# Kernel tuning notes

Measured on AMD Instinct MI355X. Metric: run time of the kernel, lower is better.

Reference implementation:

```python
import jax, jax.numpy as jnp
import numpy as np

N, C, H, D, K = 16384, 256, 8, 64, 8
HID, OUT, NE = 512, 64, 64
COMMIT, RADIUS, RHID = 0.25, 10.0, 16


def setup_inputs() -> dict:
    key = jax.random.key(0)
    ks = jax.random.split(key, 20)
    def w(k, shape, fan_in):
        return jax.random.normal(k, shape, jnp.float32) / np.sqrt(fan_in).astype(np.float32)
    return {
        'x': jax.random.normal(ks[0], (N, C), jnp.float32),
        'coors': jax.random.normal(ks[1], (N, 3), jnp.float32) * 3.0,
        'nbr_idx': jax.random.randint(ks[2], (N, K), 0, N, jnp.int32),
        'Wq': w(ks[3], (C, H * D), C),
        'Wk': w(ks[4], (C, H * D), C),
        'Wv': w(ks[5], (C, H * D), C),
        'w_gate': w(ks[6], (C, H), C),
        'Wr1': w(ks[7], (1, RHID), 1),
        'br1': jnp.zeros((RHID,), jnp.float32),
        'Wr2': w(ks[8], (RHID, H), RHID),
        'br2': jnp.zeros((H,), jnp.float32),
        'Wo': w(ks[9], (H * D + H, C), H * D + H),
        'alpha1': jnp.float32(0.5) * jnp.ones((), jnp.float32),
        'gamma1': jnp.ones((C,), jnp.float32),
        'beta1': jnp.zeros((C,), jnp.float32),
        'Wlin': w(ks[10], (C, HID), C),
        'blin': jnp.zeros((HID,), jnp.float32),
        'alpha2': jnp.float32(0.5) * jnp.ones((), jnp.float32),
        'gamma2': jnp.ones((HID + 20,), jnp.float32),
        'beta2': jnp.zeros((HID + 20,), jnp.float32),
        'Wout': w(ks[11], (HID + 20, OUT), HID + 20),
        'bout': jnp.zeros((OUT,), jnp.float32),
        'codebook': jax.random.normal(ks[12], (NE, OUT), jnp.float32),
    }


def reference(x, coors, Wq, Wk, Wv, w_gate, Wr1, br1, Wr2, br2, Wo,
              alpha1, gamma1, beta1, Wlin, blin, alpha2, gamma2, beta2,
              Wout, bout, codebook, nbr_idx):
    # ---- SE(3)-equivariant sparse-neighbor attention (heads=8, dim_head=64, K=8) ----
    q = (x @ Wq).reshape(N, H, D)
    xn = x[nbr_idx]                                  # [N,K,C] neighbor gather
    k = (xn @ Wk).reshape(N, K, H, D)
    v = (xn @ Wv).reshape(N, K, H, D)
    rel = coors[nbr_idx] - coors[:, None, :]         # [N,K,3]
    dist = jnp.sqrt(jnp.sum(rel * rel, -1) + 1e-8)   # [N,K]
    unit = rel / dist[..., None]
    radial = jax.nn.gelu(dist[..., None] @ Wr1 + br1) @ Wr2 + br2   # [N,K,H]
    logits = jnp.einsum('nhd,nkhd->nkh', q, k) / np.float32(np.sqrt(D)) + radial
    logits = jnp.where((dist <= RADIUS)[..., None], logits, jnp.float32(-1e9))
    attn = jax.nn.softmax(logits, axis=1)            # over K neighbors
    out0 = jnp.einsum('nkh,nkhd->nhd', attn, v).reshape(N, H * D)   # degree-0
    gate = xn @ w_gate                               # [N,K,H]
    vec = jnp.einsum('nkh,nkx->nhx', attn * gate, unit)             # degree-1 [N,H,3]
    vecnorm = jnp.sqrt(jnp.sum(vec * vec, -1) + 1e-8)               # invariant [N,H]
    se3_out = x + jnp.concatenate([out0, vecnorm], -1) @ Wo         # residual
    # ---- lin: DynamicTanh -> Linear -> GELU ----
    h = jnp.tanh(alpha1 * se3_out) * gamma1 + beta1
    h = jax.nn.gelu(h @ Wlin + blin)
    # ---- out_dense: concat 20-dim aa feats, DynamicTanh -> Linear -> GELU -> Tanh ----
    h2 = jnp.concatenate([h, x[:, :20]], -1)
    h2 = jnp.tanh(alpha2 * h2) * gamma2 + beta2
    z = jnp.tanh(jax.nn.gelu(h2 @ Wout + bout))      # [N,OUT]
    # ---- VQ-EMA: nearest codebook entry, commitment loss, straight-through ----
    d2 = (jnp.sum(z * z, -1, keepdims=True)
          - 2.0 * z @ codebook.T
          + jnp.sum(codebook * codebook, -1))
    idx = jnp.argmin(d2, axis=-1)
    zq = codebook[idx]
    vq_loss = COMMIT * jnp.mean((z - jax.lax.stop_gradient(zq)) ** 2)
    z_quantized = z + jax.lax.stop_gradient(zq - z)
    return z_quantized, vq_loss
```

## Files before the change

kernel.cpp:

```cpp
#include <hip/hip_runtime.h>
#include <hip/hip_bf16.h>
#include <stdint.h>

#define NPTS 16384
#define CDIM 256
#define HEADS 8
#define KNBR 8
#define HIDD 512
#define OUTD 64
#define NEMB 64
#define RHIDD 16

typedef _Float16 half8 __attribute__((ext_vector_type(8)));
typedef float f32x4 __attribute__((ext_vector_type(4)));

__device__ __forceinline__ float gelu_tanh(float v) {
    float v3 = v * v * v;
    return 0.5f * v * (1.0f + tanhf(0.79788456080286535588f * (v + 0.044715f * v3)));
}

__device__ __forceinline__ void gload16(const void* g, void* l) {
    __builtin_amdgcn_global_load_lds((const __attribute__((address_space(1))) void*)g,
                                     (__attribute__((address_space(3))) void*)l, 16, 0, 0);
}

template <int EPI>
__launch_bounds__(256)
__global__ void gemm_split(const _Float16* __restrict__ A2, const _Float16* __restrict__ B2,
                           int Kpad, int KT,
                           void* __restrict__ Cout, int ldc,
                           const float* __restrict__ bias,
                           const float* __restrict__ res,
                           const float* __restrict__ alphap,
                           const float* __restrict__ gamma,
                           const float* __restrict__ beta,
                           const float* __restrict__ a2p,
                           const float* __restrict__ g2,
                           const float* __restrict__ b2,
                           void* __restrict__ aux) {
    __shared__ __align__(16) char lds[32768];

    const int tid = threadIdx.x;
    const int l = tid & 63, w = tid >> 6;
    const int g = l >> 4, r = l & 15;
    const int wr = w >> 1, wc = w & 1;
    const int m0 = blockIdx.y * 128;
    const int n0 = blockIdx.x * 128;
    const int ldA = 2 * Kpad;
    const int srow = l >> 3;
    const int scol = ((l & 7) ^ srow) << 3;
    const int swz = (r & 7) << 4;
    const int aBase = (wr * 64 + r) * 128;
    const int bBase = 16384 + (wc * 64 + r) * 128;

    f32x4 acc[4][4] = {};

    for (int kt = 0; kt < KT; ++kt) {
        int k0 = kt * 64;
        int term = (k0 >= Kpad) ? ((k0 >= 2 * Kpad) ? 2 : 1) : 0;
        int kk0 = k0 - term * Kpad;
        int srcA = (term < 2) ? kk0 : (Kpad + kk0);
        int srcB = (term == 1) ? (Kpad + kk0) : kk0;
        const _Float16* aS = A2 + (size_t)m0 * ldA + srcA + scol;
        const _Float16* bS = B2 + (size_t)n0 * ldA + srcB + scol;
        #pragma unroll
        for (int cc = 0; cc < 4; ++cc) {
            int ch = w * 4 + cc;
            int row = ch * 8 + srow;
            gload16(aS + (size_t)row * ldA, lds + ch * 1024);
            gload16(bS + (size_t)row * ldA, lds + 16384 + ch * 1024);
        }
        __syncthreads();
        #pragma unroll
        for (int kb = 0; kb < 2; ++kb) {
            int ko = ((kb << 6) | (g << 4)) ^ swz;
            half8 af[4], bf[4];
            #pragma unroll
            for (int i = 0; i < 4; ++i) af[i] = *(const half8*)(lds + aBase + i * 2048 + ko);
            #pragma unroll
            for (int j = 0; j < 4; ++j) bf[j] = *(const half8*)(lds + bBase + j * 2048 + ko);
            #pragma unroll
            for (int i = 0; i < 4; ++i)
                #pragma unroll
                for (int j = 0; j < 4; ++j)
                    acc[i][j] = __builtin_amdgcn_mfma_f32_16x16x32_f16(af[i], bf[j], acc[i][j], 0, 0, 0);
        }
        __syncthreads();
    }

    const float alp = (EPI == 1 || EPI == 2) ? alphap[0] : 0.f;
    #pragma unroll
    for (int i = 0; i < 4; ++i) {
        #pragma unroll
        for (int j = 0; j < 4; ++j) {
            const int gcol = n0 + wc * 64 + j * 16 + r;
            #pragma unroll
            for (int q = 0; q < 4; ++q) {
                const int row = m0 + wr * 64 + i * 16 + g * 4 + q;
                float v = acc[i][j][q];
                if (EPI == 0) {
                    if (gcol < 1536) {
                        ((float*)Cout)[(size_t)row * 1536 + gcol] = v;
                    } else if (gcol < 1544) {
                        ((float*)aux)[(size_t)row * 8 + (gcol - 1536)] = v;
                    }
                } else if (EPI == 1) {
                    v += res[(size_t)row * CDIM + gcol];
                    v = tanhf(alp * v) * gamma[gcol] + beta[gcol];
                    _Float16 hi = (_Float16)v;
                    _Float16 lo = (_Float16)(v - (float)hi);
                    _Float16* H = (_Float16*)Cout;
                    H[(size_t)row * 512 + gcol] = hi;
                    H[(size_t)row * 512 + 256 + gcol] = lo;
                    if (gcol < 64) {
                        int tc = 512 + gcol;
                        float tv = 0.f;
                        if (gcol < 20)
                            tv = tanhf(a2p[0] * res[(size_t)row * CDIM + gcol]) * g2[tc] + b2[tc];
                        _Float16 thi = (_Float16)tv;
                        _Float16 tlo = (_Float16)(tv - (float)thi);
                        _Float16* T = (_Float16*)aux;
                        T[(size_t)row * 1152 + tc] = thi;
                        T[(size_t)row * 1152 + 576 + tc] = tlo;
                    }
                } else if (EPI == 2) {
                    v = gelu_tanh(v + bias[gcol]);
                    v = tanhf(alp * v) * gamma[gcol] + beta[gcol];
                    _Float16 hi = (_Float16)v;
                    _Float16 lo = (_Float16)(v - (float)hi);
                    _Float16* H = (_Float16*)Cout;
                    H[(size_t)row * 1152 + gcol] = hi;
                    H[(size_t)row * 1152 + 576 + gcol] = lo;
                }
            }
        }
    }
}

__launch_bounds__(256)
__global__ void gemm_out_vq(const _Float16* __restrict__ A2, const _Float16* __restrict__ B2,
                            const float* __restrict__ bout, const float* __restrict__ cb,
                            float* __restrict__ outZ, float* __restrict__ partials) {
    __shared__ __align__(16) char lds[34816];
    __shared__ float psum[64];
    float* zL  = (float*)lds;
    float* cbL = (float*)(lds + 17408);

    const int tid = threadIdx.x;
    const int l = tid & 63, w = tid >> 6;
    const int g = l >> 4, r = l & 15;
    const int wr = w >> 1, wc = w & 1;
    const int m0 = blockIdx.x * 64;
    const int ldA = 1152;
    const int srow = l >> 3;
    const int scol = ((l & 7) ^ srow) << 3;
    const int swz = (r & 7) << 4;
    const int aBase = (wr * 32 + r) * 128;
    const int bBase = 8192 + (wc * 32 + r) * 128;

    f32x4 acc[2][2] = {};

    for (int kt = 0; kt < 27; ++kt) {
        int k0 = kt * 64;
        int term = (k0 >= 576) ? ((k0 >= 1152) ? 2 : 1) : 0;
        int kk0 = k0 - term * 576;
        int srcA = (term < 2) ? kk0 : (576 + kk0);
        int srcB = (term == 1) ? (576 + kk0) : kk0;
        const _Float16* aS = A2 + (size_t)m0 * ldA + srcA + scol;
        const _Float16* bS = B2 + srcB + scol;
        #pragma unroll
        for (int cc = 0; cc < 2; ++cc) {
            int ch = w * 2 + cc;
            int row = ch * 8 + srow;
            gload16(aS + (size_t)row * ldA, lds + ch * 1024);
            gload16(bS + (size_t)row * ldA, lds + 8192 + ch * 1024);
        }
        __syncthreads();
        #pragma unroll
        for (int kb = 0; kb < 2; ++kb) {
            int ko = ((kb << 6) | (g << 4)) ^ swz;
            half8 af[2], bf[2];
            #pragma unroll
            for (int i = 0; i < 2; ++i) af[i] = *(const half8*)(lds + aBase + i * 2048 + ko);
            #pragma unroll
            for (int j = 0; j < 2; ++j) bf[j] = *(const half8*)(lds + bBase + j * 2048 + ko);
            #pragma unroll
            for (int i = 0; i < 2; ++i)
                #pragma unroll
                for (int j = 0; j < 2; ++j)
                    acc[i][j] = __builtin_amdgcn_mfma_f32_16x16x32_f16(af[i], bf[j], acc[i][j], 0, 0, 0);
        }
        __syncthreads();
    }

    #pragma unroll
    for (int i = 0; i < 2; ++i) {
        #pragma unroll
        for (int j = 0; j < 2; ++j) {
            int col = wc * 32 + j * 16 + r;
            #pragma unroll
            for (int q = 0; q < 4; ++q) {
                int rl = wr * 32 + i * 16 + g * 4 + q;
                zL[rl * 68 + col] = tanhf(gelu_tanh(acc[i][j][q] + bout[col]));
            }
        }
    }
    for (int i = tid; i < NEMB * OUTD / 4; i += 256) {
        float4 v = ((const float4*)cb)[i];
        int e = (i * 4) >> 6, c0 = (i * 4) & 63;
        cbL[e * 68 + c0 + 0] = v.x; cbL[e * 68 + c0 + 1] = v.y;
        cbL[e * 68 + c0 + 2] = v.z; cbL[e * 68 + c0 + 3] = v.w;
    }
    __syncthreads();
    if (tid < 64) {
        float cc = 0.f;
        #pragma unroll
        for (int d = 0; d < 64; ++d) { float cv = cbL[tid * 68 + d]; cc += cv * cv; }
        cbL[tid * 68 + 64] = cc;
    }
    __syncthreads();

    const int row = tid >> 2, part = tid & 3;
    float best = 1e30f;
    int bidx = 0;
    for (int e = part * 16; e < part * 16 + 16; ++e) {
        float dot = 0.f;
        #pragma unroll
        for (int d = 0; d < 64; ++d) dot += zL[row * 68 + d] * cbL[e * 68 + d];
        float sc = cbL[e * 68 + 64] - 2.f * dot;
        if (sc < best) { best = sc; bidx = e; }
    }
    #pragma unroll
    for (int m = 1; m <= 2; m <<= 1) {
        float ob = __shfl_xor(best, m, 64);
        int oi = __shfl_xor(bidx, m, 64);
        if (ob < best || (ob == best && oi < bidx)) { best = ob; bidx = oi; }
    }
    const int grow = m0 + row;
    float lsum = 0.f;
    #pragma unroll
    for (int u = 0; u < 16; ++u) {
        float cv = cbL[bidx * 68 + part * 16 + u];
        outZ[(size_t)grow * 64 + part * 16 + u] = cv;
        float df = zL[row * 68 + part * 16 + u] - cv;
        lsum += df * df;
    }
    lsum += __shfl_xor(lsum, 1, 64);
    lsum += __shfl_xor(lsum, 2, 64);
    if (part == 0) psum[row] = lsum;
    __syncthreads();
    if (tid < 64) {
        float v = psum[tid];
        #pragma unroll
        for (int m = 1; m < 64; m <<= 1) v += __shfl_xor(v, m, 64);
        if (tid == 0) partials[blockIdx.x] = v;
    }
}

__global__ void vq_reduce(const float* __restrict__ partials, float* __restrict__ out) {
    __shared__ float s[256];
    int tid = threadIdx.x;
    s[tid] = partials[tid];
    __syncthreads();
    for (int st = 128; st > 0; st >>= 1) {
        if (tid < st) s[tid] += s[tid + st];
        __syncthreads();
    }
    if (tid == 0) out[0] = 0.25f * s[0] / ((float)NPTS * (float)OUTD);
}

#define R0 (NPTS * CDIM)
#define S1 (1664 * 256)
#define S2 (256 * 576)
#define S3 (512 * 256)
#define S4 (64 * 576)
__global__ void prep(const float* __restrict__ x,
                     const float* __restrict__ Wq, const float* __restrict__ Wk,
                     const float* __restrict__ Wv, const float* __restrict__ w_gate,
                     const float* __restrict__ Wo, const float* __restrict__ Wlin,
                     const float* __restrict__ Wout,
                     _Float16* __restrict__ x2, _Float16* __restrict__ wqkv2,
                     _Float16* __restrict__ wo2, _Float16* __restrict__ wlin2,
                     _Float16* __restrict__ wout2) {
    for (int idx = blockIdx.x * 256 + threadIdx.x; idx < R0 + S1 + S2 + S3 + S4;
         idx += gridDim.x * 256) {
        float v; _Float16* dst; size_t o0, o1;
        if (idx < R0) {
            int n = idx >> 8, cc = idx & 255;
            v = x[idx];
            dst = x2; o0 = (size_t)n * 512 + cc; o1 = o0 + 256;
        } else if (idx < R0 + S1) {
            int t = idx - R0;
            int j = t >> 8, k = t & 255;
            if (j < 1536) {
                int jm = j & 511;
                const float* W = (j < 512) ? Wq : (j < 1024) ? Wk : Wv;
                v = W[(size_t)k * 512 + jm];
            } else if (j < 1544) {
                v = w_gate[(size_t)k * 8 + (j - 1536)];
            } else {
                v = 0.f;
            }
            dst = wqkv2; o0 = (size_t)j * 512 + k; o1 = o0 + 256;
        } else if (idx < R0 + S1 + S2) {
            int t = idx - R0 - S1;
            int j = t / 576, k = t - j * 576;
            v = (k < 520) ? Wo[(size_t)k * 256 + j] : 0.f;
            dst = wo2; o0 = (size_t)j * 1152 + k; o1 = o0 + 576;
        } else if (idx < R0 + S1 + S2 + S3) {
            int t = idx - R0 - S1 - S2;
            int j = t >> 8, k = t & 255;
            v = Wlin[(size_t)k * 512 + j];
            dst = wlin2; o0 = (size_t)j * 512 + k; o1 = o0 + 256;
        } else {
            int t = idx - R0 - S1 - S2 - S3;
            int j = t / 576, k = t - j * 576;
            v = (k < 532) ? Wout[(size_t)k * 64 + j] : 0.f;
            dst = wout2; o0 = (size_t)j * 1152 + k; o1 = o0 + 576;
        }
        _Float16 hi = (_Float16)v, lo = (_Float16)(v - (float)hi);
        dst[o0] = hi; dst[o1] = lo;
    }
}

__launch_bounds__(256)
__global__ void attn_kernel(const float* __restrict__ QKV, const float* __restrict__ G,
                            const float* __restrict__ coors, const int* __restrict__ nbr,
                            const float* __restrict__ Wr1, const float* __restrict__ br1,
                            const float* __restrict__ Wr2, const float* __restrict__ br2,
                            _Float16* __restrict__ att2) {
    __shared__ float unitL[4][8][3];
    __shared__ float distL[4][8];
    __shared__ float radH[4][8][16];

    const int tid = threadIdx.x;
    const int w = tid >> 6;
    const int lane = tid & 63;
    const int n = blockIdx.x * 4 + w;
    const int h = lane >> 3;
    const int c = lane & 7;

    int jreg[KNBR];
    #pragma unroll
    for (int k = 0; k < KNBR; ++k) jreg[k] = nbr[(size_t)n * KNBR + k];

    if (lane < KNBR) {
        int jj = jreg[lane];
        float rx = coors[(size_t)jj * 3 + 0] - coors[(size_t)n * 3 + 0];
        float ry = coors[(size_t)jj * 3 + 1] - coors[(size_t)n * 3 + 1];
        float rz = coors[(size_t)jj * 3 + 2] - coors[(size_t)n * 3 + 2];
        float d = sqrtf(rx * rx + ry * ry + rz * rz + 1e-8f);
        float inv = 1.0f / d;
        distL[w][lane] = d;
        unitL[w][lane][0] = rx * inv;
        unitL[w][lane][1] = ry * inv;
        unitL[w][lane][2] = rz * inv;
    }

    const float4* qp = (const float4*)(QKV + (size_t)n * 1536 + lane * 8);
    float4 q0 = qp[0], q1 = qp[1];
    float p[KNBR];
    #pragma unroll
    for (int k = 0; k < KNBR; ++k) {
        const float4* kp = (const float4*)(QKV + (size_t)jreg[k] * 1536 + 512 + lane * 8);
        float4 k0 = kp[0], k1 = kp[1];
        p[k] = q0.x * k0.x + q0.y * k0.y + q0.z * k0.z + q0.w * k0.w
             + q1.x * k1.x + q1.y * k1.y + q1.z * k1.z + q1.w * k1.w;
    }
    #pragma unroll
    for (int m = 1; m <= 4; m <<= 1) {
        #pragma unroll
        for (int k = 0; k < KNBR; ++k) p[k] += __shfl_xor(p[k], m, 64);
    }
    __syncthreads();

    #pragma unroll
    for (int rr = 0; rr < 2; ++rr) {
        int idx = lane + rr * 64;
        int k = idx >> 4, i = idx & 15;
        float hv = distL[w][k] * Wr1[i] + br1[i];
        radH[w][k][i] = gelu_tanh(hv);
    }
    __syncthreads();

    float lg[KNBR];
    float b2v = br2[h];
    #pragma unroll
    for (int k = 0; k < KNBR; ++k) {
        float rad = b2v;
        #pragma unroll
        for (int i = 0; i < RHIDD; ++i) rad += radH[w][k][i] * Wr2[i * HEADS + h];
        lg[k] = p[k] * 0.125f + rad;
        if (!(distL[w][k] <= 10.0f)) lg[k] = -1e9f;
    }
    float mx = lg[0];
    #pragma unroll
    for (int k = 1; k < KNBR; ++k) mx = fmaxf(mx, lg[k]);
    float a[KNBR];
    float s = 0.f;
    #pragma unroll
    for (int k = 0; k < KNBR; ++k) { a[k] = expf(lg[k] - mx); s += a[k]; }
    float is = 1.0f / s;
    #pragma unroll
    for (int k = 0; k < KNBR; ++k) a[k] *= is;

    float vx = 0.f, vy = 0.f, vz = 0.f;
    #pragma unroll
    for (int k = 0; k < KNBR; ++k) {
        float gg = G[(size_t)jreg[k] * HEADS + h];
        float ag = a[k] * gg;
        vx += ag * unitL[w][k][0];
        vy += ag * unitL[w][k][1];
        vz += ag * unitL[w][k][2];
    }
    float vn = sqrtf(vx * vx + vy * vy + vz * vz + 1e-8f);

    float4 o0 = {0.f, 0.f, 0.f, 0.f}, o1 = {0.f, 0.f, 0.f, 0.f};
    #pragma unroll
    for (int k = 0; k < KNBR; ++k) {
        const float4* vp = (const float4*)(QKV + (size_t)jreg[k] * 1536 + 1024 + lane * 8);
        float4 v0 = vp[0], v1 = vp[1];
        float ak = a[k];
        o0.x += ak * v0.x; o0.y += ak * v0.y; o0.z += ak * v0.z; o0.w += ak * v0.w;
        o1.x += ak * v1.x; o1.y += ak * v1.y; o1.z += ak * v1.z; o1.w += ak * v1.w;
    }

    float ov[8] = {o0.x, o0.y, o0.z, o0.w, o1.x, o1.y, o1.z, o1.w};
    half8 hi8, lo8;
    #pragma unroll
    for (int t = 0; t < 8; ++t) {
        _Float16 hi = (_Float16)ov[t];
        hi8[t] = hi;
        lo8[t] = (_Float16)(ov[t] - (float)hi);
    }
    *(half8*)(att2 + (size_t)n * 1152 + lane * 8) = hi8;
    *(half8*)(att2 + (size_t)n * 1152 + 576 + lane * 8) = lo8;
    if (c == 0) {
        _Float16 hi = (_Float16)vn, lo = (_Float16)(vn - (float)hi);
        att2[(size_t)n * 1152 + 512 + h] = hi;
        att2[(size_t)n * 1152 + 576 + 512 + h] = lo;
    }
    if (lane < 56) {
        att2[(size_t)n * 1152 + 520 + lane] = (_Float16)0.f;
        att2[(size_t)n * 1152 + 1096 + lane] = (_Float16)0.f;
    }
}

extern "C" void kernel_launch(void* const* d_in, const int* in_sizes, int n_in,
                              void* d_out, int out_size, void* d_ws, size_t ws_size,
                              hipStream_t stream) {
    const float* x      = (const float*)d_in[0];
    const float* coors  = (const float*)d_in[1];
    const int*   nbr    = (const int*)  d_in[2];
    const float* Wq     = (const float*)d_in[3];
    const float* Wk     = (const float*)d_in[4];
    const float* Wv     = (const float*)d_in[5];
    const float* w_gate = (const float*)d_in[6];
    const float* Wr1    = (const float*)d_in[7];
    const float* br1    = (const float*)d_in[8];
    const float* Wr2    = (const float*)d_in[9];
    const float* br2    = (const float*)d_in[10];
    const float* Wo     = (const float*)d_in[11];
    const float* alpha1 = (const float*)d_in[12];
    const float* gamma1 = (const float*)d_in[13];
    const float* beta1  = (const float*)d_in[14];
    const float* Wlin   = (const float*)d_in[15];
    const float* blin   = (const float*)d_in[16];
    const float* alpha2 = (const float*)d_in[17];
    const float* gamma2 = (const float*)d_in[18];
    const float* beta2  = (const float*)d_in[19];
    const float* Wout   = (const float*)d_in[20];
    const float* bout   = (const float*)d_in[21];
    const float* cb     = (const float*)d_in[22];

    char* wsb = (char*)d_ws;
    float*    QKV   = (float*)   (wsb + 0);
    _Float16* att2  = (_Float16*)(wsb + 100663296);
    _Float16* x2    = (_Float16*)(wsb + 138412032);
    _Float16* wqkv2 = (_Float16*)(wsb + 155189248);
    _Float16* wo2   = (_Float16*)(wsb + 156893184);
    _Float16* wlin2 = (_Float16*)(wsb + 157483008);
    _Float16* wout2 = (_Float16*)(wsb + 158007296);
    float*    G     = (float*)   (wsb + 158154752);
    float*    part  = (float*)   (wsb + 158679040);
    _Float16* h1s   = (_Float16*)(wsb + 0);
    _Float16* h2s   = (_Float16*)(wsb + 20299776);

    float* outZ    = (float*)d_out;
    float* outLoss = outZ + (size_t)NPTS * OUTD;

    dim3 blk(256);

    prep<<<dim3(2048), blk, 0, stream>>>(x, Wq, Wk, Wv, w_gate, Wo, Wlin, Wout,
                                         x2, wqkv2, wo2, wlin2, wout2);
    gemm_split<0><<<dim3(13, 128), blk, 0, stream>>>(x2, wqkv2, 256, 12, QKV, 1536,
        nullptr, nullptr, nullptr, nullptr, nullptr, nullptr, nullptr, nullptr, G);
    attn_kernel<<<dim3(NPTS / 4), blk, 0, stream>>>(QKV, G, coors, nbr, Wr1, br1, Wr2, br2, att2);
    gemm_split<1><<<dim3(2, 128), blk, 0, stream>>>(att2, wo2, 576, 27, h1s, 0,
        nullptr, x, alpha1, gamma1, beta1, alpha2, gamma2, beta2, h2s);
    gemm_split<2><<<dim3(4, 128), blk, 0, stream>>>(h1s, wlin2, 256, 12, h2s, 0,
        blin, nullptr, alpha2, gamma2, beta2, nullptr, nullptr, nullptr, nullptr);
    gemm_out_vq<<<dim3(256), blk, 0, stream>>>(h2s, wout2, bout, cb, outZ, part);
    vq_reduce<<<dim3(1), blk, 0, stream>>>(part, outLoss);
}
```

Measured before the change: 426.8 us.

## Load hi and lo split-fp16 halves into one tile and reuse fragments

```diff
diff --git a/kernel.cpp b/kernel.cpp
--- a/kernel.cpp
+++ b/kernel.cpp
@@ -48,43 +48,53 @@
     const int n0 = blockIdx.x * 128;
     const int ldA = 2 * Kpad;
     const int srow = l >> 3;
-    const int scol = ((l & 7) ^ srow) << 3;
-    const int swz = (r & 7) << 4;
+    const int sl = (l & 7) ^ srow;
+    const int scol = (sl & 3) * 8 + ((sl >= 4) ? Kpad : 0);
+    const int swz = (l & 7) << 4;
     const int aBase = (wr * 64 + r) * 128;
     const int bBase = 16384 + (wc * 64 + r) * 128;
+    const int koh = (g << 4) ^ swz;
+    const int kol = (64 | (g << 4)) ^ swz;
 
     f32x4 acc[4][4] = {};
 
-    for (int kt = 0; kt < KT; ++kt) {
-        int k0 = kt * 64;
-        int term = (k0 >= Kpad) ? ((k0 >= 2 * Kpad) ? 2 : 1) : 0;
-        int kk0 = k0 - term * Kpad;
-        int srcA = (term < 2) ? kk0 : (Kpad + kk0);
-        int srcB = (term == 1) ? (Kpad + kk0) : kk0;
-        const _Float16* aS = A2 + (size_t)m0 * ldA + srcA + scol;
-        const _Float16* bS = B2 + (size_t)n0 * ldA + srcB + scol;
+    const _Float16* aS = A2 + (size_t)m0 * ldA + scol;
+    const _Float16* bS = B2 + (size_t)n0 * ldA + scol;
+
+    for (int t = 0; t < KT; ++t) {
+        const int kk = t * 32;
         #pragma unroll
         for (int cc = 0; cc < 4; ++cc) {
             int ch = w * 4 + cc;
             int row = ch * 8 + srow;
-            gload16(aS + (size_t)row * ldA, lds + ch * 1024);
-            gload16(bS + (size_t)row * ldA, lds + 16384 + ch * 1024);
+            gload16(aS + (size_t)row * ldA + kk, lds + ch * 1024);
+            gload16(bS + (size_t)row * ldA + kk, lds + 16384 + ch * 1024);
         }
         __syncthreads();
-        #pragma unroll
-        for (int kb = 0; kb < 2; ++kb) {
-            int ko = ((kb << 6) | (g << 4)) ^ swz;
-            half8 af[4], bf[4];
-            #pragma unroll
-            for (int i = 0; i < 4; ++i) af[i] = *(const half8*)(lds + aBase + i * 2048 + ko);
-            #pragma unroll
-            for (int j = 0; j < 4; ++j) bf[j] = *(const half8*)(lds + bBase + j * 2048 + ko);
-            #pragma unroll
-            for (int i = 0; i < 4; ++i)
-                #pragma unroll
-                for (int j = 0; j < 4; ++j)
-                    acc[i][j] = __builtin_amdgcn_mfma_f32_16x16x32_f16(af[i], bf[j], acc[i][j], 0, 0, 0);
-        }
+        half8 ah[4], bh[4], xf[4];
+        #pragma unroll
+        for (int i = 0; i < 4; ++i) ah[i] = *(const half8*)(lds + aBase + i * 2048 + koh);
+        #pragma unroll
+        for (int j = 0; j < 4; ++j) bh[j] = *(const half8*)(lds + bBase + j * 2048 + koh);
+        #pragma unroll
+        for (int i = 0; i < 4; ++i)
+            #pragma unroll
+            for (int j = 0; j < 4; ++j)
+                acc[i][j] = __builtin_amdgcn_mfma_f32_16x16x32_f16(ah[i], bh[j], acc[i][j], 0, 0, 0);
+        #pragma unroll
+        for (int j = 0; j < 4; ++j) xf[j] = *(const half8*)(lds + bBase + j * 2048 + kol);
+        #pragma unroll
+        for (int i = 0; i < 4; ++i)
+            #pragma unroll
+            for (int j = 0; j < 4; ++j)
+                acc[i][j] = __builtin_amdgcn_mfma_f32_16x16x32_f16(ah[i], xf[j], acc[i][j], 0, 0, 0);
+        #pragma unroll
+        for (int i = 0; i < 4; ++i) xf[i] = *(const half8*)(lds + aBase + i * 2048 + kol);
+        #pragma unroll
+        for (int i = 0; i < 4; ++i)
+            #pragma unroll
+            for (int j = 0; j < 4; ++j)
+                acc[i][j] = __builtin_amdgcn_mfma_f32_16x16x32_f16(xf[i], bh[j], acc[i][j], 0, 0, 0);
         __syncthreads();
     }
 
@@ -151,45 +161,56 @@
     const int g = l >> 4, r = l & 15;
     const int wr = w >> 1, wc = w & 1;
     const int m0 = blockIdx.x * 64;
+    const int Kpad = 576;
     const int ldA = 1152;
     const int srow = l >> 3;
-    const int scol = ((l & 7) ^ srow) << 3;
-    const int swz = (r & 7) << 4;
+    const int sl = (l & 7) ^ srow;
+    const int scol = (sl & 3) * 8 + ((sl >= 4) ? Kpad : 0);
+    const int swz = (l & 7) << 4;
     const int aBase = (wr * 32 + r) * 128;
     const int bBase = 8192 + (wc * 32 + r) * 128;
+    const int koh = (g << 4) ^ swz;
+    const int kol = (64 | (g << 4)) ^ swz;
 
     f32x4 acc[2][2] = {};
 
-    for (int kt = 0; kt < 27; ++kt) {
-        int k0 = kt * 64;
-        int term = (k0 >= 576) ? ((k0 >= 1152) ? 2 : 1) : 0;
-        int kk0 = k0 - term * 576;
-        int srcA = (term < 2) ? kk0 : (576 + kk0);
-        int srcB = (term == 1) ? (576 + kk0) : kk0;
-        const _Float16* aS = A2 + (size_t)m0 * ldA + srcA + scol;
-        const _Float16* bS = B2 + srcB + scol;
+    const _Float16* aS = A2 + (size_t)m0 * ldA + scol;
+    const _Float16* bS = B2 + scol;
+
+    for (int t = 0; t < 18; ++t) {
+        const int kk = t * 32;
         #pragma unroll
         for (int cc = 0; cc < 2; ++cc) {
             int ch = w * 2 + cc;
             int row = ch * 8 + srow;
-            gload16(aS + (size_t)row * ldA, lds + ch * 1024);
-            gload16(bS + (size_t)row * ldA, lds + 8192 + ch * 1024);
+            gload16(aS + (size_t)row * ldA + kk, lds + ch * 1024);
+            gload16(bS + (size_t)row * ldA + kk, lds + 8192 + ch * 1024);
         }
         __syncthreads();
-        #pragma unroll
-        for (int kb = 0; kb < 2; ++kb) {
-            int ko = ((kb << 6) | (g << 4)) ^ swz;
-            half8 af[2], bf[2];
-            #pragma unroll
-            for (int i = 0; i < 2; ++i) af[i] = *(const half8*)(lds + aBase + i * 2048 + ko);
-            #pragma unroll
-            for (int j = 0; j < 2; ++j) bf[j] = *(const half8*)(lds + bBase + j * 2048 + ko);
-            #pragma unroll
-            for (int i = 0; i < 2; ++i)
-                #pragma unroll
-                for (int j = 0; j < 2; ++j)
-                    acc[i][j] = __builtin_amdgcn_mfma_f32_16x16x32_f16(af[i], bf[j], acc[i][j], 0, 0, 0);
-        }
+        half8 ah[2], bh[2], xf[2];
+        #pragma unroll
+        for (int i = 0; i < 2; ++i) ah[i] = *(const half8*)(lds + aBase + i * 2048 + koh);
+        #pragma unroll
+        for (int j = 0; j < 2; ++j) bh[j] = *(const half8*)(lds + bBase + j * 2048 + koh);
+        #pragma unroll
+        for (int i = 0; i < 2; ++i)
+            #pragma unroll
+            for (int j = 0; j < 2; ++j)
+                acc[i][j] = __builtin_amdgcn_mfma_f32_16x16x32_f16(ah[i], bh[j], acc[i][j], 0, 0, 0);
+        #pragma unroll
+        for (int j = 0; j < 2; ++j) xf[j] = *(const half8*)(lds + bBase + j * 2048 + kol);
+        #pragma unroll
+        for (int i = 0; i < 2; ++i)
+            #pragma unroll
+            for (int j = 0; j < 2; ++j)
+                acc[i][j] = __builtin_amdgcn_mfma_f32_16x16x32_f16(ah[i], xf[j], acc[i][j], 0, 0, 0);
+        #pragma unroll
+        for (int i = 0; i < 2; ++i) xf[i] = *(const half8*)(lds + aBase + i * 2048 + kol);
+        #pragma unroll
+        for (int i = 0; i < 2; ++i)
+            #pragma unroll
+            for (int j = 0; j < 2; ++j)
+                acc[i][j] = __builtin_amdgcn_mfma_f32_16x16x32_f16(xf[i], bh[j], acc[i][j], 0, 0, 0);
         __syncthreads();
     }
 
@@ -493,12 +514,12 @@
 
     prep<<<dim3(2048), blk, 0, stream>>>(x, Wq, Wk, Wv, w_gate, Wo, Wlin, Wout,
                                          x2, wqkv2, wo2, wlin2, wout2);
-    gemm_split<0><<<dim3(13, 128), blk, 0, stream>>>(x2, wqkv2, 256, 12, QKV, 1536,
+    gemm_split<0><<<dim3(13, 128), blk, 0, stream>>>(x2, wqkv2, 256, 8, QKV, 1536,
         nullptr, nullptr, nullptr, nullptr, nullptr, nullptr, nullptr, nullptr, G);
     attn_kernel<<<dim3(NPTS / 4), blk, 0, stream>>>(QKV, G, coors, nbr, Wr1, br1, Wr2, br2, att2);
-    gemm_split<1><<<dim3(2, 128), blk, 0, stream>>>(att2, wo2, 576, 27, h1s, 0,
+    gemm_split<1><<<dim3(2, 128), blk, 0, stream>>>(att2, wo2, 576, 18, h1s, 0,
         nullptr, x, alpha1, gamma1, beta1, alpha2, gamma2, beta2, h2s);
-    gemm_split<2><<<dim3(4, 128), blk, 0, stream>>>(h1s, wlin2, 256, 12, h2s, 0,
+    gemm_split<2><<<dim3(4, 128), blk, 0, stream>>>(h1s, wlin2, 256, 8, h2s, 0,
         blin, nullptr, alpha2, gamma2, beta2, nullptr, nullptr, nullptr, nullptr);
     gemm_out_vq<<<dim3(256), blk, 0, stream>>>(h2s, wout2, bout, cb, outZ, part);
     vq_reduce<<<dim3(1), blk, 0, stream>>>(part, outLoss);
```

Measured after the change: 397.8 us. 1.07x faster.
